# Optimization experiments

Hardware: AMD Instinct MI355X
Metric: run time of the kernel (lower is better)

The kernel has to match this reference:

```python
import jax, jax.numpy as jnp
import numpy as np

# Acoustic FDTD constants (seistorch-style geometry)
NSHOTS, NT = 4, 512
NZ, NX = 256, 256
NRECS = 128
DT = 1e-3   # s
DH = 10.0   # m grid spacing


def setup_inputs() -> dict:
    key = jax.random.key(0)
    k1, k2, k3, k4, k5, k6 = jax.random.split(key, 6)
    x = jax.random.normal(k1, (NSHOTS, NT), dtype=jnp.float32)  # source wavelets
    # velocity model in [1500, 4000] m/s (CFL: dt*vmax/dh = 0.4 < stability limit)
    vp = 1500.0 + 2500.0 * jax.random.uniform(k2, (NZ, NX), dtype=jnp.float32)
    src_z = jax.random.randint(k3, (NSHOTS,), 0, NZ)
    src_x = jax.random.randint(k4, (NSHOTS,), 0, NX)
    rec_z = jax.random.randint(k5, (NSHOTS, NRECS), 0, NZ)
    rec_x = jax.random.randint(k6, (NSHOTS, NRECS), 0, NX)
    return {"x": x, "vp": vp, "src_z": src_z, "src_x": src_x,
            "rec_z": rec_z, "rec_x": rec_x}


def _laplacian(p):
    # 5-point stencil, zero Dirichlet boundary. p: (B, NZ, NX)
    pp = jnp.pad(p, ((0, 0), (1, 1), (1, 1)))
    return (pp[:, 2:, 1:-1] + pp[:, :-2, 1:-1]
            + pp[:, 1:-1, 2:] + pp[:, 1:-1, :-2]
            - 4.0 * p) / (DH * DH)


def reference(x, vp, src_z, src_x, rec_z, rec_x):
    shots = jnp.arange(NSHOTS)
    c2dt2 = (vp * DT) ** 2  # (NZ, NX), broadcast over shots

    def step(carry, wav_t):
        p_prev, p = carry
        # 2nd-order acoustic update (the PDE "cell")
        p_next = 2.0 * p - p_prev + c2dt2 * _laplacian(p)
        # source scatter-inject (super_source)
        p_next = p_next.at[shots, src_z, src_x].add(wav_t * DT * DT)
        # receiver gather (super_probes): (NSHOTS, NRECS)
        rec = p_next[shots[:, None], rec_z, rec_x]
        return (p, p_next), rec

    p0 = jnp.zeros((NSHOTS, NZ, NX), dtype=x.dtype)
    _, recs = jax.lax.scan(step, (p0, p0), x.T)  # recs: (NT, NSHOTS, NRECS)
    # (shots, time, receivers, n_receiver_types=1)
    return jnp.transpose(recs, (1, 0, 2))[..., None]
```

## Files before the change

kernel.cpp:

```cpp
#include <hip/hip_runtime.h>

#define NSHOTS 4
#define NT     512
#define NZ     256
#define NX     256
#define NRECS  128

static constexpr float DTf    = 0.001f;
static constexpr float INVDH2 = 1.0f / (10.0f * 10.0f);

#define KSTEPS 16
#define TILE   32
#define RPT    8
#define NPAIRS 4
#define NWAVES 8
#define BLOCK  512
#define NWG    (NSHOTS * 64)
#define NPHASE (NT / KSTEPS)

typedef float v2f __attribute__((ext_vector_type(2)));
typedef unsigned long long ull;

__device__ __forceinline__ float nbr_left(float v) {
  return __int_as_float(__builtin_amdgcn_update_dpp(
      0, __float_as_int(v), 0x138 , 0xf, 0xf, true));
}
__device__ __forceinline__ float nbr_right(float v) {
  return __int_as_float(__builtin_amdgcn_update_dpp(
      0, __float_as_int(v), 0x130 , 0xf, 0xf, true));
}

__device__ __forceinline__ ull pload(const ull* p) {
  return __hip_atomic_load(p, __ATOMIC_RELAXED, __HIP_MEMORY_SCOPE_AGENT);
}
__device__ __forceinline__ void pstore(ull* p, ull v) {
  __hip_atomic_store(p, v, __ATOMIC_RELAXED, __HIP_MEMORY_SCOPE_AGENT);
}

__device__ __forceinline__ ull pack_w(float cur, float prev, unsigned tg) {
  const unsigned hi = (__float_as_uint(prev) & ~3u) | tg;
  return ((ull)hi << 32) | (ull)__float_as_uint(cur);
}
__device__ __forceinline__ float w_cur(ull w) {
  return __uint_as_float((unsigned)w);
}
__device__ __forceinline__ float w_prev(ull w) {
  return __uint_as_float(((unsigned)(w >> 32)) & ~3u);
}
__device__ __forceinline__ unsigned tag_of(int q) {
  return ((unsigned)(q >> 1) % 3u) + 1u;
}

__global__ __launch_bounds__(BLOCK, 4) void wave_pk(
    ull* __restrict__ gA, ull* __restrict__ gB,
    const float* __restrict__ vp, const float* __restrict__ xwav,
    const int* __restrict__ src_z, const int* __restrict__ src_x,
    const int* __restrict__ rec_z, const int* __restrict__ rec_x,
    float* __restrict__ out)
{
  const int bid  = blockIdx.x;
  const int s    = bid >> 6;
  const int tz   = (bid >> 3) & 7;
  const int tx   = bid & 7;
  const int tid  = threadIdx.x;
  const int w    = tid >> 6;
  const int lane = tid & 63;

  const int gz0 = tz * TILE - KSTEPS;
  const int gx0 = tx * TILE - KSTEPS;
  const int gx  = gx0 + lane;
  const int zb  = w * RPT;

  __shared__ float haloTop[2][NWAVES][64];
  __shared__ float haloBot[2][NWAVES][64];
  __shared__ int   lzA[NRECS], lxA[NRECS];

  if (tid < NRECS) {
    lzA[tid] = rec_z[s * NRECS + tid] - tz * TILE;
    lxA[tid] = rec_x[s * NRECS + tid] - tx * TILE;
  }
  __syncthreads();

  const bool wbRow = (w >= 2 && w < 6) && (lane >= KSTEPS && lane < KSTEPS + TILE);

  unsigned e0 = 0, e1 = 0, ov[4] = {0, 0, 0, 0};
  if (wbRow) {
    int cnt = 0;
    #pragma unroll 1
    for (int r = 0; r < NRECS; ++r) {
      const int lz = lzA[r], lx = lxA[r];
      if ((unsigned)lz < (unsigned)TILE && (unsigned)lx < (unsigned)TILE) {
        const int ez = lz + KSTEPS;
        if ((ez >> 3) == w && lx + KSTEPS == lane) {
          const unsigned e = 0x8000u | ((unsigned)(ez & 7) << 8) | (unsigned)r;
          if (cnt == 0) e0 = e;
          else if (cnt == 1) e1 = e;
          else ov[r >> 5] |= 1u << (r & 31);
          ++cnt;
        }
      }
    }
  }
  const bool hasOvf = (ov[0] | ov[1] | ov[2] | ov[3]) != 0;

  const int slz = src_z[s] - gz0;
  const int slx = src_x[s] - gx0;
  const bool srcMine = (slx == lane) && ((unsigned)(slz - zb) < (unsigned)RPT);
  const int  srcI = slz - zb;
  v2f srcM2[NPAIRS];
  #pragma unroll
  for (int p = 0; p < NPAIRS; ++p) {
    srcM2[p].x = (srcMine && srcI == 2 * p)     ? 1.0f : 0.0f;
    srcM2[p].y = (srcMine && srcI == 2 * p + 1) ? 1.0f : 0.0f;
  }

  const bool xok = (unsigned)gx < (unsigned)NX;
  int   offRow[RPT];
  bool  okRow[RPT];
  v2f a2[NPAIRS], b2[NPAIRS], c22[NPAIRS], d22[NPAIRS];
  unsigned okMask = 0;
  #pragma unroll
  for (int p = 0; p < NPAIRS; ++p) {
    #pragma unroll
    for (int h = 0; h < 2; ++h) {
      const int i  = 2 * p + h;
      const int gz = gz0 + zb + i;
      const bool ok = xok && ((unsigned)gz < (unsigned)NZ);
      okRow[i]  = ok;
      if (ok) okMask |= 1u << i;
      offRow[i] = ok ? ((s * NZ + gz) * NX + gx) : 0;
      float v = ok ? vp[gz * NX + gx] : 0.0f;
      v *= DTf;
      const float c2 = v * v * INVDH2;
      if (h == 0) { c22[p].x = c2; d22[p].x = 2.0f - 4.0f * c2; }
      else        { c22[p].y = c2; d22[p].y = 2.0f - 4.0f * c2; }
    }
    a2[p] = (v2f)(0.0f); b2[p] = (v2f)(0.0f);
  }

  auto selRow = [](const v2f (&n)[NPAIRS], int row) -> float {
    const v2f pA = (row & 2) ? n[1] : n[0];
    const v2f pB = (row & 2) ? n[3] : n[2];
    const v2f pp = (row & 4) ? pB : pA;
    return (row & 1) ? pp.y : pp.x;
  };

  #pragma unroll 1
  for (int ph = 0; ph < NPHASE; ++ph) {
    const int t0 = ph * KSTEPS;

    float amp[KSTEPS];
    {
      const float4* xw4 = (const float4*)(xwav + s * NT + t0);
      #pragma unroll
      for (int q = 0; q < KSTEPS / 4; ++q) {
        const float4 v = xw4[q];
        amp[4 * q + 0] = (v.x * DTf) * DTf;
        amp[4 * q + 1] = (v.y * DTf) * DTf;
        amp[4 * q + 2] = (v.z * DTf) * DTf;
        amp[4 * q + 3] = (v.w * DTf) * DTf;
      }
    }

    if (ph > 0 && !wbRow) {
      const ull* gR = (ph & 1) ? gA : gB;
      const unsigned tg = tag_of(ph - 1);
      ull vw[RPT];
      unsigned need = okMask;
      while (need) {
        ull t[RPT];
        #pragma unroll
        for (int i = 0; i < RPT; ++i)
          if (need & (1u << i)) t[i] = pload(gR + offRow[i]);
        #pragma unroll
        for (int i = 0; i < RPT; ++i)
          if ((need & (1u << i)) && (((unsigned)(t[i] >> 32)) & 3u) == tg) {
            vw[i] = t[i];
            need &= ~(1u << i);
          }
        if (need) __builtin_amdgcn_s_sleep(1);
      }
      #pragma unroll
      for (int i = 0; i < RPT; ++i) {
        const float cv = okRow[i] ? w_cur(vw[i])  : 0.0f;
        const float pv = okRow[i] ? w_prev(vw[i]) : 0.0f;
        if (i & 1) { a2[i >> 1].y = cv; b2[i >> 1].y = pv; }
        else       { a2[i >> 1].x = cv; b2[i >> 1].x = pv; }
      }
    }

    auto do_step = [&](v2f (&cur)[NPAIRS], v2f (&nxt)[NPAIRS], int tau) {
      const int pb = tau & 1;
      haloTop[pb][w][lane] = cur[0].x;
      haloBot[pb][w][lane] = cur[NPAIRS - 1].y;
      __syncthreads();
      const float up0 = (w > 0)          ? haloBot[pb][w - 1][lane] : 0.0f;
      const float dn7 = (w < NWAVES - 1) ? haloTop[pb][w + 1][lane] : 0.0f;
      const v2f av = { amp[tau], amp[tau] };
      #pragma unroll
      for (int p = 0; p < NPAIRS; ++p) {
        const float cx = cur[p].x, cy = cur[p].y;
        const float upx = (p == 0)          ? up0 : cur[p - 1].y;
        const float dny = (p == NPAIRS - 1) ? dn7 : cur[p + 1].x;
        v2f ud, lr;
        ud.x = upx + cy;
        ud.y = cx + dny;
        lr.x = nbr_left(cx) + nbr_right(cx);
        lr.y = nbr_left(cy) + nbr_right(cy);
        const v2f sum = ud + lr;
        v2f t = __builtin_elementwise_fma(c22[p], sum, -nxt[p]);
        t = __builtin_elementwise_fma(d22[p], cur[p], t);
        t = __builtin_elementwise_fma(srcM2[p], av, t);
        nxt[p] = t;
      }
      const int t = t0 + tau;
      if (e0 & 0x8000u)
        out[(s * NT + t) * NRECS + (e0 & 127u)] = selRow(nxt, (e0 >> 8) & 7);
      if (e1 & 0x8000u)
        out[(s * NT + t) * NRECS + (e1 & 127u)] = selRow(nxt, (e1 >> 8) & 7);
      if (hasOvf) {
        #pragma unroll
        for (int wd = 0; wd < 4; ++wd) {
          unsigned m = ov[wd];
          while (m) {
            const int b = __builtin_ctz(m); m &= m - 1;
            const int r = wd * 32 + b;
            out[(s * NT + t) * NRECS + r] = selRow(nxt, (lzA[r] + KSTEPS) & 7);
          }
        }
      }
    };

    #pragma unroll
    for (int h = 0; h < KSTEPS / 2; ++h) {
      do_step(a2, b2, 2 * h);
      do_step(b2, a2, 2 * h + 1);
    }

    if (ph != NPHASE - 1 && wbRow) {
      ull* gW = (ph & 1) ? gB : gA;
      const unsigned tgw = tag_of(ph);
      #pragma unroll
      for (int p = 0; p < NPAIRS; ++p) {
        pstore(gW + offRow[2 * p],     pack_w(a2[p].x, b2[p].x, tgw));
        pstore(gW + offRow[2 * p + 1], pack_w(a2[p].y, b2[p].y, tgw));
      }
    }
  }
}

extern "C" void kernel_launch(void* const* d_in, const int* in_sizes, int n_in,
                              void* d_out, int out_size, void* d_ws, size_t ws_size,
                              hipStream_t stream) {
  const float* x     = (const float*)d_in[0];
  const float* vp    = (const float*)d_in[1];
  const int*   src_z = (const int*)d_in[2];
  const int*   src_x = (const int*)d_in[3];
  const int*   rec_z = (const int*)d_in[4];
  const int*   rec_x = (const int*)d_in[5];
  float* out = (float*)d_out;

  const size_t F = (size_t)NSHOTS * NZ * NX;
  ull* gA = (ull*)d_ws;
  ull* gB = gA + F;

  hipMemsetAsync(gA, 0, 2 * F * sizeof(ull), stream);

  wave_pk<<<dim3(NWG), dim3(BLOCK), 0, stream>>>(
      gA, gB, vp, x, src_z, src_x, rec_z, rec_x, out);
}
```

Before: 320.2 us.

## Retile wavefield into 8x48 tiles with 8-step phases across more workgroups

Replaces the 32x32 tile / 16-step temporal-blocking scheme with 8x48 interior tiles and 8 steps per phase, using 384-thread blocks and 768 workgroups instead of 256. The aim is to put several workgroups on each CU so more waves are available to hide latency, while keeping halo redundancy similar. Source-amplitude loading and injection now run only in waves that hold the source. The cost is twice as many inter-tile exchange phases through the tagged global buffers, plus more spin-waiting between neighbouring tiles.

```diff
diff --git a/kernel.cpp b/kernel.cpp
--- a/kernel.cpp
+++ b/kernel.cpp
@@ -9,14 +9,18 @@
 static constexpr float DTf    = 0.001f;
 static constexpr float INVDH2 = 1.0f / (10.0f * 10.0f);
 
-#define KSTEPS 16
-#define TILE   32
-#define RPT    8
-#define NPAIRS 4
-#define NWAVES 8
-#define BLOCK  512
-#define NWG    (NSHOTS * 64)
-#define NPHASE (NT / KSTEPS)
+#define KS     8
+#define TZI    8
+#define TXI    48
+#define EXTZ   24
+#define NW     6
+#define RPW    4
+#define NPAIRS 2
+#define BLOCK  384
+#define NTZ    32
+#define NTX    6
+#define NTILES (NSHOTS*NTZ*NTX)
+#define NPH    (NT/KS)
 
 typedef float v2f __attribute__((ext_vector_type(2)));
 typedef unsigned long long ull;
@@ -51,7 +55,7 @@
   return ((unsigned)(q >> 1) % 3u) + 1u;
 }
 
-__global__ __launch_bounds__(BLOCK, 4) void wave_pk(
+__global__ __launch_bounds__(BLOCK, 5) void wave_pk(
     ull* __restrict__ gA, ull* __restrict__ gB,
     const float* __restrict__ vp, const float* __restrict__ xwav,
     const int* __restrict__ src_z, const int* __restrict__ src_x,
@@ -59,40 +63,40 @@
     float* __restrict__ out)
 {
   const int bid  = blockIdx.x;
-  const int s    = bid >> 6;
-  const int tz   = (bid >> 3) & 7;
-  const int tx   = bid & 7;
+  const int s    = bid / (NTZ * NTX);
+  const int rem  = bid - s * (NTZ * NTX);
+  const int tz   = rem / NTX;
+  const int tx   = rem - tz * NTX;
   const int tid  = threadIdx.x;
   const int w    = tid >> 6;
   const int lane = tid & 63;
 
-  const int gz0 = tz * TILE - KSTEPS;
-  const int gx0 = tx * TILE - KSTEPS;
+  const int gz0 = tz * TZI - KS;
+  const int gx0 = tx * TXI - KS;
   const int gx  = gx0 + lane;
-  const int zb  = w * RPT;
-
-  __shared__ float haloTop[2][NWAVES][64];
-  __shared__ float haloBot[2][NWAVES][64];
+  const int zb  = w * RPW;
+
+  __shared__ float haloTop[2][NW][64];
+  __shared__ float haloBot[2][NW][64];
   __shared__ int   lzA[NRECS], lxA[NRECS];
 
   if (tid < NRECS) {
-    lzA[tid] = rec_z[s * NRECS + tid] - tz * TILE;
-    lxA[tid] = rec_x[s * NRECS + tid] - tx * TILE;
+    lzA[tid] = rec_z[s * NRECS + tid] - tz * TZI;
+    lxA[tid] = rec_x[s * NRECS + tid] - tx * TXI;
   }
   __syncthreads();
 
-  const bool wbRow = (w >= 2 && w < 6) && (lane >= KSTEPS && lane < KSTEPS + TILE);
+  const bool wbT = (w == 2 || w == 3) && (lane >= KS && lane < KS + TXI);
 
   unsigned e0 = 0, e1 = 0, ov[4] = {0, 0, 0, 0};
-  if (wbRow) {
+  if (wbT) {
     int cnt = 0;
     #pragma unroll 1
     for (int r = 0; r < NRECS; ++r) {
       const int lz = lzA[r], lx = lxA[r];
-      if ((unsigned)lz < (unsigned)TILE && (unsigned)lx < (unsigned)TILE) {
-        const int ez = lz + KSTEPS;
-        if ((ez >> 3) == w && lx + KSTEPS == lane) {
-          const unsigned e = 0x8000u | ((unsigned)(ez & 7) << 8) | (unsigned)r;
+      if ((unsigned)lz < (unsigned)TZI && (unsigned)lx < (unsigned)TXI) {
+        if ((2 + (lz >> 2)) == w && lx + KS == lane) {
+          const unsigned e = 0x8000u | ((unsigned)(lz & 3) << 8) | (unsigned)r;
           if (cnt == 0) e0 = e;
           else if (cnt == 1) e1 = e;
           else ov[r >> 5] |= 1u << (r & 31);
@@ -105,18 +109,19 @@
 
   const int slz = src_z[s] - gz0;
   const int slx = src_x[s] - gx0;
-  const bool srcMine = (slx == lane) && ((unsigned)(slz - zb) < (unsigned)RPT);
-  const int  srcI = slz - zb;
+  const int si  = slz - zb;
+  const bool hasSrcW = ((unsigned)slx < 64u) && ((unsigned)si < (unsigned)RPW);
+  const bool srcMine = hasSrcW && (slx == lane);
   v2f srcM2[NPAIRS];
   #pragma unroll
   for (int p = 0; p < NPAIRS; ++p) {
-    srcM2[p].x = (srcMine && srcI == 2 * p)     ? 1.0f : 0.0f;
-    srcM2[p].y = (srcMine && srcI == 2 * p + 1) ? 1.0f : 0.0f;
+    srcM2[p].x = (srcMine && si == 2 * p)     ? 1.0f : 0.0f;
+    srcM2[p].y = (srcMine && si == 2 * p + 1) ? 1.0f : 0.0f;
   }
 
   const bool xok = (unsigned)gx < (unsigned)NX;
-  int   offRow[RPT];
-  bool  okRow[RPT];
+  int   offRow[RPW];
+  bool  okRow[RPW];
   v2f a2[NPAIRS], b2[NPAIRS], c22[NPAIRS], d22[NPAIRS];
   unsigned okMask = 0;
   #pragma unroll
@@ -139,41 +144,37 @@
   }
 
   auto selRow = [](const v2f (&n)[NPAIRS], int row) -> float {
-    const v2f pA = (row & 2) ? n[1] : n[0];
-    const v2f pB = (row & 2) ? n[3] : n[2];
-    const v2f pp = (row & 4) ? pB : pA;
+    const v2f pp = (row & 2) ? n[1] : n[0];
     return (row & 1) ? pp.y : pp.x;
   };
 
+  float amp[KS];
+
   #pragma unroll 1
-  for (int ph = 0; ph < NPHASE; ++ph) {
-    const int t0 = ph * KSTEPS;
-
-    float amp[KSTEPS];
-    {
-      const float4* xw4 = (const float4*)(xwav + s * NT + t0);
-      #pragma unroll
-      for (int q = 0; q < KSTEPS / 4; ++q) {
-        const float4 v = xw4[q];
-        amp[4 * q + 0] = (v.x * DTf) * DTf;
-        amp[4 * q + 1] = (v.y * DTf) * DTf;
-        amp[4 * q + 2] = (v.z * DTf) * DTf;
-        amp[4 * q + 3] = (v.w * DTf) * DTf;
-      }
-    }
-
-    if (ph > 0 && !wbRow) {
+  for (int ph = 0; ph < NPH; ++ph) {
+    const int t0 = ph * KS;
+
+    if (hasSrcW) {
+      const float4 v  = *(const float4*)(xwav + s * NT + t0);
+      const float4 u4 = *(const float4*)(xwav + s * NT + t0 + 4);
+      amp[0] = v.x * DTf * DTf;  amp[1] = v.y * DTf * DTf;
+      amp[2] = v.z * DTf * DTf;  amp[3] = v.w * DTf * DTf;
+      amp[4] = u4.x * DTf * DTf; amp[5] = u4.y * DTf * DTf;
+      amp[6] = u4.z * DTf * DTf; amp[7] = u4.w * DTf * DTf;
+    }
+
+    if (ph > 0 && !wbT) {
       const ull* gR = (ph & 1) ? gA : gB;
       const unsigned tg = tag_of(ph - 1);
-      ull vw[RPT];
+      ull vw[RPW];
       unsigned need = okMask;
       while (need) {
-        ull t[RPT];
-        #pragma unroll
-        for (int i = 0; i < RPT; ++i)
+        ull t[RPW];
+        #pragma unroll
+        for (int i = 0; i < RPW; ++i)
           if (need & (1u << i)) t[i] = pload(gR + offRow[i]);
         #pragma unroll
-        for (int i = 0; i < RPT; ++i)
+        for (int i = 0; i < RPW; ++i)
           if ((need & (1u << i)) && (((unsigned)(t[i] >> 32)) & 3u) == tg) {
             vw[i] = t[i];
             need &= ~(1u << i);
@@ -181,7 +182,7 @@
         if (need) __builtin_amdgcn_s_sleep(1);
       }
       #pragma unroll
-      for (int i = 0; i < RPT; ++i) {
+      for (int i = 0; i < RPW; ++i) {
         const float cv = okRow[i] ? w_cur(vw[i])  : 0.0f;
         const float pv = okRow[i] ? w_prev(vw[i]) : 0.0f;
         if (i & 1) { a2[i >> 1].y = cv; b2[i >> 1].y = pv; }
@@ -194,14 +195,13 @@
       haloTop[pb][w][lane] = cur[0].x;
       haloBot[pb][w][lane] = cur[NPAIRS - 1].y;
       __syncthreads();
-      const float up0 = (w > 0)          ? haloBot[pb][w - 1][lane] : 0.0f;
-      const float dn7 = (w < NWAVES - 1) ? haloTop[pb][w + 1][lane] : 0.0f;
-      const v2f av = { amp[tau], amp[tau] };
+      const float up0 = (w > 0)      ? haloBot[pb][w - 1][lane] : 0.0f;
+      const float dn  = (w < NW - 1) ? haloTop[pb][w + 1][lane] : 0.0f;
       #pragma unroll
       for (int p = 0; p < NPAIRS; ++p) {
         const float cx = cur[p].x, cy = cur[p].y;
         const float upx = (p == 0)          ? up0 : cur[p - 1].y;
-        const float dny = (p == NPAIRS - 1) ? dn7 : cur[p + 1].x;
+        const float dny = (p == NPAIRS - 1) ? dn  : cur[p + 1].x;
         v2f ud, lr;
         ud.x = upx + cy;
         ud.y = cx + dny;
@@ -210,14 +210,19 @@
         const v2f sum = ud + lr;
         v2f t = __builtin_elementwise_fma(c22[p], sum, -nxt[p]);
         t = __builtin_elementwise_fma(d22[p], cur[p], t);
-        t = __builtin_elementwise_fma(srcM2[p], av, t);
         nxt[p] = t;
+      }
+      if (hasSrcW) {
+        const v2f av = { amp[tau], amp[tau] };
+        #pragma unroll
+        for (int p = 0; p < NPAIRS; ++p)
+          nxt[p] = __builtin_elementwise_fma(srcM2[p], av, nxt[p]);
       }
       const int t = t0 + tau;
       if (e0 & 0x8000u)
-        out[(s * NT + t) * NRECS + (e0 & 127u)] = selRow(nxt, (e0 >> 8) & 7);
+        out[(s * NT + t) * NRECS + (e0 & 127u)] = selRow(nxt, (e0 >> 8) & 3);
       if (e1 & 0x8000u)
-        out[(s * NT + t) * NRECS + (e1 & 127u)] = selRow(nxt, (e1 >> 8) & 7);
+        out[(s * NT + t) * NRECS + (e1 & 127u)] = selRow(nxt, (e1 >> 8) & 3);
       if (hasOvf) {
         #pragma unroll
         for (int wd = 0; wd < 4; ++wd) {
@@ -225,26 +230,28 @@
           while (m) {
             const int b = __builtin_ctz(m); m &= m - 1;
             const int r = wd * 32 + b;
-            out[(s * NT + t) * NRECS + r] = selRow(nxt, (lzA[r] + KSTEPS) & 7);
+            out[(s * NT + t) * NRECS + r] = selRow(nxt, lzA[r] & 3);
           }
         }
       }
     };
 
     #pragma unroll
-    for (int h = 0; h < KSTEPS / 2; ++h) {
+    for (int h = 0; h < KS / 2; ++h) {
       do_step(a2, b2, 2 * h);
       do_step(b2, a2, 2 * h + 1);
     }
 
-    if (ph != NPHASE - 1 && wbRow) {
+    if (ph != NPH - 1 && wbT) {
       ull* gW = (ph & 1) ? gB : gA;
       const unsigned tgw = tag_of(ph);
       #pragma unroll
-      for (int p = 0; p < NPAIRS; ++p) {
-        pstore(gW + offRow[2 * p],     pack_w(a2[p].x, b2[p].x, tgw));
-        pstore(gW + offRow[2 * p + 1], pack_w(a2[p].y, b2[p].y, tgw));
-      }
+      for (int i = 0; i < RPW; ++i)
+        if (okRow[i]) {
+          const float cv = (i & 1) ? a2[i >> 1].y : a2[i >> 1].x;
+          const float pv = (i & 1) ? b2[i >> 1].y : b2[i >> 1].x;
+          pstore(gW + offRow[i], pack_w(cv, pv, tgw));
+        }
     }
   }
 }
@@ -266,6 +273,6 @@
 
   hipMemsetAsync(gA, 0, 2 * F * sizeof(ull), stream);
 
-  wave_pk<<<dim3(NWG), dim3(BLOCK), 0, stream>>>(
+  wave_pk<<<dim3(NTILES), dim3(BLOCK), 0, stream>>>(
       gA, gB, vp, x, src_z, src_x, rec_z, rec_x, out);
 }
```

Measured after the change: 369.4 us. +15.3%, slower.
